# Kernel tuning notes

Hardware: AMD Instinct MI355X
Metric: run time of the kernel (lower is better)

## Reference

```python
import jax, jax.numpy as jnp
import numpy as np
import math

L = 4096
D = 1280
H = 16
HD = D // H  # 80
NSEG = 4


def setup_inputs() -> dict:
    key = jax.random.key(0)
    ks = jax.random.split(key, 8)
    x = jax.random.normal(ks[0], (L, D), dtype=jnp.float32)
    cu_seqlens = jnp.array([0, 1024, 2048, 3072, 4096], dtype=jnp.int32)
    rotary_pos_emb = jax.random.uniform(ks[1], (L, HD // 2), dtype=jnp.float32) * (2 * math.pi)
    s = 1.0 / math.sqrt(D)
    W_qkv = jax.random.normal(ks[2], (3 * D, D), dtype=jnp.float32) * s
    b_qkv = jax.random.normal(ks[3], (3 * D,), dtype=jnp.float32) * 0.01
    W_proj = jax.random.normal(ks[4], (D, D), dtype=jnp.float32) * s
    b_proj = jax.random.normal(ks[5], (D,), dtype=jnp.float32) * 0.01
    return {"x": x, "cu_seqlens": cu_seqlens, "rotary_pos_emb": rotary_pos_emb,
            "W_qkv": W_qkv, "b_qkv": b_qkv, "W_proj": W_proj, "b_proj": b_proj}


def _rotary_half(t):
    t1, t2 = jnp.split(t, 2, axis=-1)
    return jnp.concatenate([-t2, t1], axis=-1)


def _apply_rope(t, freq):
    # t: (L, H, HD), freq: (L, HD/2)
    cos = jnp.concatenate([jnp.cos(freq), jnp.cos(freq)], axis=-1)[:, None, :]
    sin = jnp.concatenate([jnp.sin(freq), jnp.sin(freq)], axis=-1)[:, None, :]
    return t * cos + _rotary_half(t) * sin


def reference(x, cu_seqlens, rotary_pos_emb, W_qkv, b_qkv, W_proj, b_proj):
    seq_len = x.shape[0]
    qkv = (x @ W_qkv.T + b_qkv).reshape(seq_len, 3, H, HD)
    q, k, v = qkv[:, 0], qkv[:, 1], qkv[:, 2]  # each (L, H, HD)
    q = _apply_rope(q, rotary_pos_emb)
    k = _apply_rope(k, rotary_pos_emb)
    # scores: (H, L, L)
    scores = jnp.einsum('lhd,mhd->hlm', q, k) / math.sqrt(HD)
    # block-diagonal mask from cu_seqlens: same segment -> 0, else finfo.min
    seg = jnp.searchsorted(cu_seqlens, jnp.arange(seq_len, dtype=jnp.int32), side='right')  # (L,)
    same = seg[:, None] == seg[None, :]
    neg = jnp.finfo(scores.dtype).min
    scores = scores + jnp.where(same, jnp.array(0.0, scores.dtype), neg)[None, :, :]
    attn = jax.nn.softmax(scores.astype(jnp.float32), axis=-1).astype(q.dtype)
    out = jnp.einsum('hlm,mhd->lhd', attn, v).reshape(seq_len, D)
    return out @ W_proj.T + b_proj
```

## Files before the change

kernel.cpp:

```cpp
#include <hip/hip_runtime.h>
#include <hip/hip_bf16.h>
#include <math.h>

#define LL   4096
#define DD   1280
#define HH   16
#define HDD  80
#define QKVN (3 * DD)

typedef __attribute__((ext_vector_type(8))) short sv8;
typedef __attribute__((ext_vector_type(4))) short sv4;
typedef __attribute__((ext_vector_type(4))) float fv4;

#if __has_builtin(__builtin_amdgcn_mfma_f32_16x16x16bf16_1k)
#define MFMA16(a, b, c) __builtin_amdgcn_mfma_f32_16x16x16bf16_1k(a, b, c, 0, 0, 0)
#elif __has_builtin(__builtin_amdgcn_mfma_f32_16x16x16_bf16)
#define MFMA16(a, b, c) __builtin_amdgcn_mfma_f32_16x16x16_bf16(a, b, c, 0, 0, 0)
#else
__device__ static inline fv4 MFMA16(sv4, sv4, fv4 c) { return c; }
#endif

#if __has_builtin(__builtin_amdgcn_exp2f)
#define EXP2F(x) __builtin_amdgcn_exp2f(x)
#else
#define EXP2F(x) exp2f(x)
#endif

#define SETPRIO(n) __builtin_amdgcn_s_setprio(n)
#define SCHEDB()   __builtin_amdgcn_sched_barrier(0)

static __device__ __forceinline__ unsigned short f2bf(float f) {
  unsigned int u = __builtin_bit_cast(unsigned int, f);
  u += 0x7FFF + ((u >> 16) & 1);
  return (unsigned short)(u >> 16);
}
static __device__ __forceinline__ float bf2f(unsigned short b) {
  unsigned int u = ((unsigned int)b) << 16;
  return __builtin_bit_cast(float, u);
}
static __device__ __forceinline__ unsigned int cvt_pk_bf16(float lo, float hi) {
  __hip_bfloat162 h = __float22bfloat162_rn(make_float2(lo, hi));
  unsigned int u;
  __builtin_memcpy(&u, &h, 4);
  return u;
}

#define GLD_LDS(gsrc, ldst)                                                          \
  __builtin_amdgcn_global_load_lds(                                                  \
      (const __attribute__((address_space(1))) unsigned int*)(gsrc),                 \
      (__attribute__((address_space(3))) unsigned int*)(ldst), 16, 0, 0)

__global__ __launch_bounds__(256) void cast3_kernel(
    const float* __restrict__ x, const float* __restrict__ w1,
    const float* __restrict__ w2, unsigned short* __restrict__ xb,
    unsigned short* __restrict__ w1b, unsigned short* __restrict__ w2b) {
  const int n0 = LL * DD / 8, n1 = QKVN * DD / 8, n2 = DD * DD / 8;
  int i = blockIdx.x * 256 + threadIdx.x;
  const float* in; unsigned short* out; int j;
  if (i < n0)           { in = x;  out = xb;  j = i; }
  else if (i < n0 + n1) { in = w1; out = w1b; j = i - n0; }
  else if (i < n0 + n1 + n2) { in = w2; out = w2b; j = i - n0 - n1; }
  else return;
  const float4* p = (const float4*)(in + (size_t)j * 8);
  float4 v0 = p[0], v1 = p[1];
  union { sv8 v; unsigned int u[4]; } o;
  o.u[0] = cvt_pk_bf16(v0.x, v0.y);
  o.u[1] = cvt_pk_bf16(v0.z, v0.w);
  o.u[2] = cvt_pk_bf16(v1.x, v1.y);
  o.u[3] = cvt_pk_bf16(v1.z, v1.w);
  *(sv8*)(out + (size_t)j * 8) = o.v;
}

__global__ __launch_bounds__(512, 2) void gemm256_bf16_kernel(
    const unsigned short* __restrict__ A, const unsigned short* __restrict__ B,
    const float* __restrict__ bias, unsigned short* __restrict__ C,
    unsigned short* __restrict__ Vp, int M, int N, int K) {
  __shared__ __attribute__((aligned(16))) unsigned short As[3][256 * 32];
  __shared__ __attribute__((aligned(16))) unsigned short Bs[3][256 * 32];
  int tid = threadIdx.x, w = tid >> 6, lane = tid & 63;
  int g = lane >> 4, l15 = lane & 15;
  int wr = w >> 2, wc = w & 3;

  int bid = blockIdx.x;
  int wg = (bid & 7) * 30 + (bid >> 3);
  int bm = (wg / 15) * 256;
  int bn = (wg % 15) * 256;

  fv4 acc[8][4];
#pragma unroll
  for (int a = 0; a < 8; ++a)
#pragma unroll
    for (int b = 0; b < 4; ++b) acc[a][b] = (fv4){0.f, 0.f, 0.f, 0.f};

  auto STAGE = [&](int buf, int t) {
    int k0 = t * 32;
#pragma unroll
    for (int i = 0; i < 4; ++i) {
      int cid = w * 4 + i;
      int c = cid & 15;
      int row = c * 16 + (lane >> 2);
      int gsrc = (lane & 3) ^ ((row >> 1) & 3);
      const unsigned short* src = (cid < 16)
          ? A + (size_t)(bm + row) * K + k0 + gsrc * 8
          : B + (size_t)(bn + row) * K + k0 + gsrc * 8;
      unsigned short* dst = ((cid < 16) ? As[buf] : Bs[buf]) + c * 512;
      GLD_LDS(src, dst);
    }
  };

  const int NT = 40;
  int r = 0;
  STAGE(0, 0);
  STAGE(1, 1);
  for (int t = 0; t < NT; ++t) {
    if (t + 1 < NT) asm volatile("s_waitcnt vmcnt(4)" ::: "memory");
    else            asm volatile("s_waitcnt vmcnt(0)" ::: "memory");
    SCHEDB();
    asm volatile("s_barrier" ::: "memory");
    int s2 = (r == 0) ? 2 : r - 1;
    if (t + 2 < NT) STAGE(s2, t + 2);

    const unsigned short* Ab = As[r];
    const unsigned short* Bb = Bs[r];
    sv8 af[4], bfr[4];
#pragma unroll
    for (int nt = 0; nt < 4; ++nt) {
      int row = wc * 64 + nt * 16 + l15;
      bfr[nt] = *(const sv8*)(Bb + row * 32 + ((g ^ ((row >> 1) & 3)) * 8));
    }
#pragma unroll
    for (int mt = 0; mt < 4; ++mt) {
      int row = wr * 128 + mt * 16 + l15;
      af[mt] = *(const sv8*)(Ab + row * 32 + ((g ^ ((row >> 1) & 3)) * 8));
    }
    SCHEDB();
    SETPRIO(1);
#pragma unroll
    for (int mt = 0; mt < 4; ++mt)
#pragma unroll
      for (int nt = 0; nt < 4; ++nt)
        acc[mt][nt] = __builtin_amdgcn_mfma_f32_16x16x32_bf16(af[mt], bfr[nt], acc[mt][nt], 0, 0, 0);
    SETPRIO(0);
    SCHEDB();
    sv8 af2[4];
#pragma unroll
    for (int mt = 0; mt < 4; ++mt) {
      int row = wr * 128 + (mt + 4) * 16 + l15;
      af2[mt] = *(const sv8*)(Ab + row * 32 + ((g ^ ((row >> 1) & 3)) * 8));
    }
    SCHEDB();
    SETPRIO(1);
#pragma unroll
    for (int mt = 0; mt < 4; ++mt)
#pragma unroll
      for (int nt = 0; nt < 4; ++nt)
        acc[mt + 4][nt] = __builtin_amdgcn_mfma_f32_16x16x32_bf16(af2[mt], bfr[nt], acc[mt + 4][nt], 0, 0, 0);
    SETPRIO(0);
    r = (r == 2) ? 0 : r + 1;
  }

  if (bn < 2560) {
#pragma unroll
    for (int mt = 0; mt < 8; ++mt)
#pragma unroll
      for (int nt = 0; nt < 4; ++nt) {
        int n = bn + wc * 64 + nt * 16 + l15;
        float bv = bias[n];
#pragma unroll
        for (int rr = 0; rr < 4; ++rr) {
          int m = bm + wr * 128 + mt * 16 + 4 * g + rr;
          C[(size_t)m * N + n] = f2bf(acc[mt][nt][rr] + bv);
        }
      }
  } else {
#pragma unroll
    for (int mt = 0; mt < 8; ++mt)
#pragma unroll
      for (int nt = 0; nt < 4; ++nt) {
        int n = bn + wc * 64 + nt * 16 + l15;
        int v = n - 2560;
        int h = v / HDD, d = v % HDD;
        float bv = bias[n];
        int m0 = bm + wr * 128 + mt * 16 + 4 * g;
        int blk = m0 >> 6, ntg = (m0 >> 2) & 15;
        uint2 pk;
        pk.x = cvt_pk_bf16(acc[mt][nt][0] + bv, acc[mt][nt][1] + bv);
        pk.y = cvt_pk_bf16(acc[mt][nt][2] + bv, acc[mt][nt][3] + bv);
        size_t unit = (((size_t)h * 64 + blk) * 16 + ntg) * HDD + d;
        *(uint2*)(Vp + unit * 4) = pk;
      }
  }
}

__global__ __launch_bounds__(256) void gemm_bf16_kernel(
    const unsigned short* __restrict__ A, const unsigned short* __restrict__ B,
    const float* __restrict__ bias, void* __restrict__ Cv,
    int M, int N, int K, int out_bf16) {
  __shared__ __attribute__((aligned(16))) unsigned short As[2][128 * 64];
  __shared__ __attribute__((aligned(16))) unsigned short Bs[2][128 * 64];
  int tid = threadIdx.x, w = tid >> 6, lane = tid & 63;
  int g = lane >> 4, l15 = lane & 15;
  int wr = w >> 1, wc = w & 1;
  int bm = blockIdx.y * 128, bn = blockIdx.x * 128;

  fv4 acc[4][4];
#pragma unroll
  for (int a = 0; a < 4; ++a)
#pragma unroll
    for (int b = 0; b < 4; ++b) acc[a][b] = (fv4){0.f, 0.f, 0.f, 0.f};

  auto STAGE = [&](int buf, int k0) {
#pragma unroll
    for (int i = 0; i < 4; ++i) {
      int c = w * 4 + i;
      int row = 8 * c + (lane >> 3);
      int cb = lane & 7;
      int gcol = k0 + ((cb ^ (row & 7)) * 8);
      GLD_LDS(A + (size_t)(bm + row) * K + gcol, As[buf] + c * 512);
      GLD_LDS(B + (size_t)(bn + row) * K + gcol, Bs[buf] + c * 512);
    }
  };

  int nt = K / 64, cur = 0;
  STAGE(0, 0);
  if (nt > 1) STAGE(1, 64);
  for (int t = 0; t < nt; ++t) {
    if (t + 1 < nt) asm volatile("s_waitcnt vmcnt(8)" ::: "memory");
    else            asm volatile("s_waitcnt vmcnt(0)" ::: "memory");
    SCHEDB();
    asm volatile("s_barrier" ::: "memory");
    const unsigned short* Ab = As[cur];
    const unsigned short* Bb = Bs[cur];
#pragma unroll
    for (int s = 0; s < 2; ++s) {
      sv8 af[4], bf[4];
#pragma unroll
      for (int t4 = 0; t4 < 4; ++t4) {
        int ra = wr * 64 + t4 * 16 + l15;
        af[t4] = *(const sv8*)(Ab + ra * 64 + (((s * 4 + g) ^ (ra & 7)) * 8));
        int rb = wc * 64 + t4 * 16 + l15;
        bf[t4] = *(const sv8*)(Bb + rb * 64 + (((s * 4 + g) ^ (rb & 7)) * 8));
      }
      SCHEDB();
      SETPRIO(1);
#pragma unroll
      for (int mt = 0; mt < 4; ++mt)
#pragma unroll
        for (int nt2 = 0; nt2 < 4; ++nt2)
          acc[mt][nt2] = __builtin_amdgcn_mfma_f32_16x16x32_bf16(af[mt], bf[nt2], acc[mt][nt2], 0, 0, 0);
      SETPRIO(0);
      SCHEDB();
    }
    asm volatile("s_waitcnt lgkmcnt(0)" ::: "memory");
    asm volatile("s_barrier" ::: "memory");
    if (t + 2 < nt) STAGE(cur, (t + 2) * 64);
    cur ^= 1;
  }

  if (out_bf16) {
    unsigned short* C = (unsigned short*)Cv;
#pragma unroll
    for (int mt = 0; mt < 4; ++mt)
#pragma unroll
      for (int nt2 = 0; nt2 < 4; ++nt2)
#pragma unroll
        for (int r = 0; r < 4; ++r) {
          int m = bm + wr * 64 + mt * 16 + 4 * g + r;
          int n = bn + wc * 64 + nt2 * 16 + l15;
          C[(size_t)m * N + n] = f2bf(acc[mt][nt2][r] + bias[n]);
        }
  } else {
    float* C = (float*)Cv;
#pragma unroll
    for (int mt = 0; mt < 4; ++mt)
#pragma unroll
      for (int nt2 = 0; nt2 < 4; ++nt2)
#pragma unroll
        for (int r = 0; r < 4; ++r) {
          int m = bm + wr * 64 + mt * 16 + 4 * g + r;
          int n = bn + wc * 64 + nt2 * 16 + l15;
          C[(size_t)m * N + n] = acc[mt][nt2][r] + bias[n];
        }
  }
}

__global__ __launch_bounds__(192) void pack_qk_kernel(
    const unsigned short* __restrict__ qkvb, const float* __restrict__ freqs,
    unsigned short* __restrict__ Qb, unsigned short* __restrict__ Kmain,
    unsigned short* __restrict__ Ktail) {
  int l = blockIdx.x;
  __shared__ float cs[40], sn[40];
  if (threadIdx.x < 40) {
    float f = freqs[(size_t)l * 40 + threadIdx.x];
    cs[threadIdx.x] = cosf(f);
    sn[threadIdx.x] = sinf(f);
  }
  __syncthreads();
  int t = threadIdx.x;
  if (t >= 160) return;
  int which = t / 80;
  int rem   = t % 80;
  int h = rem / 5, pg = rem % 5;
  int d0 = pg * 8;
  const unsigned short* src = qkvb + (size_t)l * QKVN + which * DD + h * HDD;
  union { sv8 v; unsigned short u[8]; } A, B;
  A.v = *(const sv8*)(src + d0);
  B.v = *(const sv8*)(src + d0 + 40);
  float scale = which ? 1.0f : 0.16129822676f;
  float lo[8], hi[8];
#pragma unroll
  for (int j = 0; j < 8; ++j) {
    float c = cs[d0 + j], s = sn[d0 + j];
    float a = bf2f(A.u[j]), b = bf2f(B.u[j]);
    lo[j] = (a * c - b * s) * scale;
    hi[j] = (b * c + a * s) * scale;
  }
  union { sv8 v; unsigned int u[4]; } OL, OH;
#pragma unroll
  for (int j = 0; j < 4; ++j) {
    OL.u[j] = cvt_pk_bf16(lo[2 * j], lo[2 * j + 1]);
    OH.u[j] = cvt_pk_bf16(hi[2 * j], hi[2 * j + 1]);
  }
  if (which == 0) {
    unsigned short* dst = Qb + ((size_t)h * LL + l) * HDD;
    *(sv8*)(dst + d0) = OL.v;
    *(sv8*)(dst + d0 + 40) = OH.v;
  } else {
    unsigned short* km = Kmain + ((size_t)h * LL + l) * 64;
    *(sv8*)(km + pg * 8) = OL.v;
    int dh = d0 + 40;
    if (dh < 64) {
      *(sv8*)(km + dh) = OH.v;
    } else {
      int blk = l >> 6, key = l & 63;
      int tg0 = (dh - 64) >> 2;
      size_t base = (((size_t)h * 64 + blk) * 4);
      uint2 w0 = make_uint2(OH.u[0], OH.u[1]);
      uint2 w1 = make_uint2(OH.u[2], OH.u[3]);
      *(uint2*)(Ktail + ((base + tg0) * 64 + key) * 4)     = w0;
      *(uint2*)(Ktail + ((base + tg0 + 1) * 64 + key) * 4) = w1;
    }
  }
}

__global__ __launch_bounds__(256) void attn_mfma_kernel(
    const unsigned short* __restrict__ Qb,
    const unsigned short* __restrict__ Kmain,
    const unsigned short* __restrict__ Ktail,
    const unsigned short* __restrict__ Vp,
    const int* __restrict__ cu,
    unsigned short* __restrict__ outb) {
  __shared__ __attribute__((aligned(16))) unsigned short Ks[2][64 * 64];
  __shared__ __attribute__((aligned(16))) unsigned short Kt[2][4 * 64 * 4];
  __shared__ __attribute__((aligned(16))) unsigned short Vl[2][16 * 80 * 4];
  int tid = threadIdx.x, w = tid >> 6, lane = tid & 63;
  int g = lane >> 4, l15 = lane & 15;

  int bid = blockIdx.x;
  int sw = (bid & 7) * 128 + (bid >> 3);
  int h = sw >> 6;
  int q0 = (sw & 63) * 64;

  int s0 = 0, s1 = LL;
#pragma unroll
  for (int i = 0; i < 4; ++i) {
    int a = cu[i], b = cu[i + 1];
    if (q0 >= a && q0 < b) { s0 = a; s1 = b; }
  }

  int qrow = q0 + w * 16 + l15;
  const unsigned short* qp = Qb + ((size_t)h * LL + qrow) * HDD;
  sv8 aq[2];
#pragma unroll
  for (int s = 0; s < 2; ++s) aq[s] = *(const sv8*)(qp + s * 32 + g * 8);
  union { sv4 v; uint2 u2; } qt;
  qt.u2 = *(const uint2*)(qp + 64 + 4 * g);

  auto STAGE = [&](int buf, int kb) {
    int blk = kb >> 6;
#pragma unroll
    for (int i = 0; i < 5; ++i) {
      int cid = w + 4 * i;
      if (cid < 8) {
        int row = 8 * cid + (lane >> 3);
        int cb = lane & 7;
        GLD_LDS(Kmain + ((size_t)h * LL + kb + row) * 64 + ((cb ^ (row & 7)) * 8),
                Ks[buf] + cid * 512);
      } else if (cid < 10) {
        int tc = cid - 8;
        GLD_LDS(Ktail + ((((size_t)h * 64 + blk) * 256) + tc * 128 + 2 * lane) * 4,
                Kt[buf] + tc * 512);
      } else {
        int vc = cid - 10;
        GLD_LDS(Vp + ((((size_t)h * 64 + blk) * 1280) + vc * 128 + 2 * lane) * 4,
                Vl[buf] + vc * 512);
      }
    }
  };

  fv4 o[5];
#pragma unroll
  for (int dt = 0; dt < 5; ++dt) o[dt] = (fv4){0.f, 0.f, 0.f, 0.f};
  float lsum = 0.f;

  int cur = 0;
  STAGE(0, s0);
  if (s0 + 64 < s1) STAGE(1, s0 + 64);
  for (int kb = s0; kb < s1; kb += 64) {
    if (kb + 64 < s1) asm volatile("s_waitcnt vmcnt(5)" ::: "memory");
    else              asm volatile("s_waitcnt vmcnt(0)" ::: "memory");
    SCHEDB();
    asm volatile("s_barrier" ::: "memory");
    const unsigned short* Kc = Ks[cur];
    const unsigned short* Ktc = Kt[cur];
    const unsigned short* Vc = Vl[cur];

    SETPRIO(1);
    fv4 sf[4];
#pragma unroll
    for (int nt = 0; nt < 4; ++nt) sf[nt] = (fv4){0.f, 0.f, 0.f, 0.f};
#pragma unroll
    for (int s = 0; s < 2; ++s) {
#pragma unroll
      for (int nt = 0; nt < 4; ++nt) {
        int key = nt * 16 + l15;
        sv8 ak = *(const sv8*)(Kc + key * 64 + (((s * 4 + g) ^ (key & 7)) * 8));
        sf[nt] = __builtin_amdgcn_mfma_f32_16x16x32_bf16(ak, aq[s], sf[nt], 0, 0, 0);
      }
    }
#pragma unroll
    for (int nt = 0; nt < 4; ++nt) {
      sv4 akt = *(const sv4*)(Ktc + (g * 64 + nt * 16 + l15) * 4);
      sf[nt] = MFMA16(akt, qt.v, sf[nt]);
    }

#pragma unroll
    for (int nt = 0; nt < 4; ++nt) {
      float p0 = EXP2F(sf[nt][0]);
      float p1 = EXP2F(sf[nt][1]);
      float p2 = EXP2F(sf[nt][2]);
      float p3 = EXP2F(sf[nt][3]);
      lsum += (p0 + p1) + (p2 + p3);
      union { sv4 v; unsigned int u[2]; } pa;
      pa.u[0] = cvt_pk_bf16(p0, p1);
      pa.u[1] = cvt_pk_bf16(p2, p3);
#pragma unroll
      for (int dt = 0; dt < 5; ++dt) {
        sv4 vb4 = *(const sv4*)(Vc + ((nt * 4 + g) * 80 + dt * 16 + l15) * 4);
        o[dt] = MFMA16(pa.v, vb4, o[dt]);
      }
    }
    SETPRIO(0);
    asm volatile("s_waitcnt lgkmcnt(0)" ::: "memory");
    asm volatile("s_barrier" ::: "memory");
    if (kb + 128 < s1) STAGE(cur, kb + 128);
    cur ^= 1;
  }

  lsum += __shfl_xor(lsum, 16);
  lsum += __shfl_xor(lsum, 32);
  float inv = 1.f / lsum;
#pragma unroll
  for (int r = 0; r < 4; ++r) {
    float invr = __shfl(inv, 4 * g + r);
    int row = q0 + w * 16 + 4 * g + r;
#pragma unroll
    for (int dt = 0; dt < 5; ++dt) {
      outb[(size_t)row * DD + h * HDD + dt * 16 + l15] = f2bf(o[dt][r] * invr);
    }
  }
}

extern "C" void kernel_launch(void* const* d_in, const int* in_sizes, int n_in,
                              void* d_out, int out_size, void* d_ws, size_t ws_size,
                              hipStream_t stream) {
  const float* x     = (const float*)d_in[0];
  const int*   cu    = (const int*)d_in[1];
  const float* rope  = (const float*)d_in[2];
  const float* Wqkv  = (const float*)d_in[3];
  const float* bqkv  = (const float*)d_in[4];
  const float* Wproj = (const float*)d_in[5];
  const float* bproj = (const float*)d_in[6];
  float* out = (float*)d_out;

  char* ws = (char*)d_ws;
  unsigned short* qkvb   = (unsigned short*)ws;
  unsigned short* attn_b = (unsigned short*)ws;
  unsigned short* xb     = (unsigned short*)(ws + 31457280);
  unsigned short* Wqkvb  = (unsigned short*)(ws + 41943040);
  unsigned short* Wprojb = (unsigned short*)(ws + 51773440);
  unsigned short* Kmain  = (unsigned short*)(ws + 55050240);
  unsigned short* Ktail  = (unsigned short*)(ws + 63438848);
  unsigned short* Vp     = (unsigned short*)(ws + 65536000);
  unsigned short* Qb     = xb;

  {
    int n8 = LL * DD / 8 + QKVN * DD / 8 + DD * DD / 8;
    cast3_kernel<<<(n8 + 255) / 256, 256, 0, stream>>>(x, Wqkv, Wproj, xb, Wqkvb, Wprojb);
  }

  gemm256_bf16_kernel<<<240, 512, 0, stream>>>(
      xb, Wqkvb, bqkv, qkvb, Vp, LL, QKVN, DD);

  pack_qk_kernel<<<LL, 192, 0, stream>>>(qkvb, rope, Qb, Kmain, Ktail);

  attn_mfma_kernel<<<1024, 256, 0, stream>>>(Qb, Kmain, Ktail, Vp, cu, attn_b);

  gemm_bf16_kernel<<<dim3(DD / 128, LL / 128), 256, 0, stream>>>(
      attn_b, Wprojb, bproj, out, LL, DD, DD, 0);
}
```

Measured before the change: 129.1 us.

## Rewrite projection GEMM with 256x128 tiles, triple buffering and XCD-aware block mapping

Replaces the generic 128x128 projection GEMM (320 blocks of 256 threads) with a specialized kernel that uses 256x128 tiles, 512 threads, BK=32 and a three-stage LDS ring. The next stage is issued right after the barrier, so one barrier per iteration replaces two. Blocks are remapped so consecutive IDs on the same XCD share rows, aiming for better L2 reuse. The 160 blocks cover 256 CUs in a single wave, trading some CU occupancy for larger tiles and deeper prefetch.

```diff
diff --git a/kernel.cpp b/kernel.cpp
--- a/kernel.cpp
+++ b/kernel.cpp
@@ -192,96 +192,106 @@
   }
 }
 
-__global__ __launch_bounds__(256) void gemm_bf16_kernel(
+__global__ __launch_bounds__(512, 2) void gemm_proj_kernel(
     const unsigned short* __restrict__ A, const unsigned short* __restrict__ B,
-    const float* __restrict__ bias, void* __restrict__ Cv,
-    int M, int N, int K, int out_bf16) {
-  __shared__ __attribute__((aligned(16))) unsigned short As[2][128 * 64];
-  __shared__ __attribute__((aligned(16))) unsigned short Bs[2][128 * 64];
+    const float* __restrict__ bias, float* __restrict__ C,
+    int M, int N, int K) {
+  __shared__ __attribute__((aligned(16))) unsigned short As[3][256 * 32];
+  __shared__ __attribute__((aligned(16))) unsigned short Bs[3][128 * 32];
   int tid = threadIdx.x, w = tid >> 6, lane = tid & 63;
   int g = lane >> 4, l15 = lane & 15;
-  int wr = w >> 1, wc = w & 1;
-  int bm = blockIdx.y * 128, bn = blockIdx.x * 128;
-
-  fv4 acc[4][4];
-#pragma unroll
-  for (int a = 0; a < 4; ++a)
-#pragma unroll
-    for (int b = 0; b < 4; ++b) acc[a][b] = (fv4){0.f, 0.f, 0.f, 0.f};
-
-  auto STAGE = [&](int buf, int k0) {
-#pragma unroll
-    for (int i = 0; i < 4; ++i) {
-      int c = w * 4 + i;
-      int row = 8 * c + (lane >> 3);
-      int cb = lane & 7;
-      int gcol = k0 + ((cb ^ (row & 7)) * 8);
-      GLD_LDS(A + (size_t)(bm + row) * K + gcol, As[buf] + c * 512);
-      GLD_LDS(B + (size_t)(bn + row) * K + gcol, Bs[buf] + c * 512);
+  int wr = w >> 2, wc = w & 3;
+
+  int bid = blockIdx.x;
+  int wg = (bid & 7) * 20 + (bid >> 3);
+  int bm = (wg / 10) * 256;
+  int bn = (wg % 10) * 128;
+
+  fv4 acc[8][2];
+#pragma unroll
+  for (int a = 0; a < 8; ++a)
+#pragma unroll
+    for (int b = 0; b < 2; ++b) acc[a][b] = (fv4){0.f, 0.f, 0.f, 0.f};
+
+  auto STAGE = [&](int buf, int t) {
+    int k0 = t * 32;
+#pragma unroll
+    for (int i = 0; i < 3; ++i) {
+      int cid = w + 8 * i;
+      int c = (cid < 16) ? cid : (cid - 16);
+      int row = c * 16 + (lane >> 2);
+      int gsrc = (lane & 3) ^ ((row >> 1) & 3);
+      const unsigned short* src = (cid < 16)
+          ? A + (size_t)(bm + row) * K + k0 + gsrc * 8
+          : B + (size_t)(bn + row) * K + k0 + gsrc * 8;
+      unsigned short* dst = ((cid < 16) ? As[buf] : Bs[buf]) + c * 512;
+      GLD_LDS(src, dst);
     }
   };
 
-  int nt = K / 64, cur = 0;
+  const int NT = 40;
+  int r = 0;
   STAGE(0, 0);
-  if (nt > 1) STAGE(1, 64);
-  for (int t = 0; t < nt; ++t) {
-    if (t + 1 < nt) asm volatile("s_waitcnt vmcnt(8)" ::: "memory");
+  STAGE(1, 1);
+  for (int t = 0; t < NT; ++t) {
+    if (t + 1 < NT) asm volatile("s_waitcnt vmcnt(3)" ::: "memory");
     else            asm volatile("s_waitcnt vmcnt(0)" ::: "memory");
     SCHEDB();
     asm volatile("s_barrier" ::: "memory");
-    const unsigned short* Ab = As[cur];
-    const unsigned short* Bb = Bs[cur];
-#pragma unroll
-    for (int s = 0; s < 2; ++s) {
-      sv8 af[4], bf[4];
-#pragma unroll
-      for (int t4 = 0; t4 < 4; ++t4) {
-        int ra = wr * 64 + t4 * 16 + l15;
-        af[t4] = *(const sv8*)(Ab + ra * 64 + (((s * 4 + g) ^ (ra & 7)) * 8));
-        int rb = wc * 64 + t4 * 16 + l15;
-        bf[t4] = *(const sv8*)(Bb + rb * 64 + (((s * 4 + g) ^ (rb & 7)) * 8));
+    int s2 = (r == 0) ? 2 : r - 1;
+    if (t + 2 < NT) STAGE(s2, t + 2);
+
+    const unsigned short* Ab = As[r];
+    const unsigned short* Bb = Bs[r];
+    sv8 af[4], bfr[2];
+#pragma unroll
+    for (int nt = 0; nt < 2; ++nt) {
+      int row = wc * 32 + nt * 16 + l15;
+      bfr[nt] = *(const sv8*)(Bb + row * 32 + ((g ^ ((row >> 1) & 3)) * 8));
+    }
+#pragma unroll
+    for (int mt = 0; mt < 4; ++mt) {
+      int row = wr * 128 + mt * 16 + l15;
+      af[mt] = *(const sv8*)(Ab + row * 32 + ((g ^ ((row >> 1) & 3)) * 8));
+    }
+    SCHEDB();
+    SETPRIO(1);
+#pragma unroll
+    for (int mt = 0; mt < 4; ++mt)
+#pragma unroll
+      for (int nt = 0; nt < 2; ++nt)
+        acc[mt][nt] = __builtin_amdgcn_mfma_f32_16x16x32_bf16(af[mt], bfr[nt], acc[mt][nt], 0, 0, 0);
+    SETPRIO(0);
+    SCHEDB();
+    sv8 af2[4];
+#pragma unroll
+    for (int mt = 0; mt < 4; ++mt) {
+      int row = wr * 128 + (mt + 4) * 16 + l15;
+      af2[mt] = *(const sv8*)(Ab + row * 32 + ((g ^ ((row >> 1) & 3)) * 8));
+    }
+    SCHEDB();
+    SETPRIO(1);
+#pragma unroll
+    for (int mt = 0; mt < 4; ++mt)
+#pragma unroll
+      for (int nt = 0; nt < 2; ++nt)
+        acc[mt + 4][nt] = __builtin_amdgcn_mfma_f32_16x16x32_bf16(af2[mt], bfr[nt], acc[mt + 4][nt], 0, 0, 0);
+    SETPRIO(0);
+    r = (r == 2) ? 0 : r + 1;
+  }
+
+#pragma unroll
+  for (int mt = 0; mt < 8; ++mt)
+#pragma unroll
+    for (int nt = 0; nt < 2; ++nt) {
+      int n = bn + wc * 32 + nt * 16 + l15;
+      float bv = bias[n];
+#pragma unroll
+      for (int rr = 0; rr < 4; ++rr) {
+        int m = bm + wr * 128 + mt * 16 + 4 * g + rr;
+        C[(size_t)m * N + n] = acc[mt][nt][rr] + bv;
       }
-      SCHEDB();
-      SETPRIO(1);
-#pragma unroll
-      for (int mt = 0; mt < 4; ++mt)
-#pragma unroll
-        for (int nt2 = 0; nt2 < 4; ++nt2)
-          acc[mt][nt2] = __builtin_amdgcn_mfma_f32_16x16x32_bf16(af[mt], bf[nt2], acc[mt][nt2], 0, 0, 0);
-      SETPRIO(0);
-      SCHEDB();
-    }
-    asm volatile("s_waitcnt lgkmcnt(0)" ::: "memory");
-    asm volatile("s_barrier" ::: "memory");
-    if (t + 2 < nt) STAGE(cur, (t + 2) * 64);
-    cur ^= 1;
-  }
-
-  if (out_bf16) {
-    unsigned short* C = (unsigned short*)Cv;
-#pragma unroll
-    for (int mt = 0; mt < 4; ++mt)
-#pragma unroll
-      for (int nt2 = 0; nt2 < 4; ++nt2)
-#pragma unroll
-        for (int r = 0; r < 4; ++r) {
-          int m = bm + wr * 64 + mt * 16 + 4 * g + r;
-          int n = bn + wc * 64 + nt2 * 16 + l15;
-          C[(size_t)m * N + n] = f2bf(acc[mt][nt2][r] + bias[n]);
-        }
-  } else {
-    float* C = (float*)Cv;
-#pragma unroll
-    for (int mt = 0; mt < 4; ++mt)
-#pragma unroll
-      for (int nt2 = 0; nt2 < 4; ++nt2)
-#pragma unroll
-        for (int r = 0; r < 4; ++r) {
-          int m = bm + wr * 64 + mt * 16 + 4 * g + r;
-          int n = bn + wc * 64 + nt2 * 16 + l15;
-          C[(size_t)m * N + n] = acc[mt][nt2][r] + bias[n];
-        }
-  }
+    }
 }
 
 __global__ __launch_bounds__(192) void pack_qk_kernel(
@@ -506,6 +516,6 @@
 
   attn_mfma_kernel<<<1024, 256, 0, stream>>>(Qb, Kmain, Ktail, Vp, cu, attn_b);
 
-  gemm_bf16_kernel<<<dim3(DD / 128, LL / 128), 256, 0, stream>>>(
-      attn_b, Wprojb, bproj, out, LL, DD, DD, 0);
-}
+  gemm_proj_kernel<<<160, 512, 0, stream>>>(
+      attn_b, Wprojb, bproj, out, LL, DD, DD);
+}
```

Measured after the change: 138.8 us. 1.08x slower.
